# Kernel tuning notes

Measured on AMD Instinct MI355X. Metric: run time of the kernel, lower is better.

## Reference

```python
import jax, jax.numpy as jnp
import numpy as np

B = 64            # batchSize
F_ENC = 2048      # encodedFeatureSize = 128 features * 16 bits
H = 8192          # hiddenLayerSize
C = 100           # numberOfClasses
K = 8             # numberOfSynapsesPerSegment
THR = K // 2      # segment activation threshold (majority of synapses active)
NSEG = 2          # numberOfSegmentsPerNeuron


def _make_synapse_matrix(key, n_neurons, prev_size):
    # exactly K random synapses per neuron, values +1/-1 with equal prob
    k_idx, k_val = jax.random.split(key)
    cols = jax.random.randint(k_idx, (n_neurons, K), 0, prev_size)
    vals = jnp.where(jax.random.bernoulli(k_val, 0.5, (n_neurons, K)), 1.0, -1.0).astype(jnp.float32)
    rows = jnp.arange(n_neurons)[:, None]
    W = jnp.zeros((n_neurons, prev_size), dtype=jnp.float32)
    return W.at[rows, cols].set(vals)


def setup_inputs() -> dict:
    key = jax.random.key(0)
    ks = jax.random.split(key, 16)
    # binary encoded input (thermometer/gray-coded bits); rand in [0,1), binarized in reference
    x = jax.random.uniform(ks[0], (B, F_ENC), dtype=jnp.float32)
    W0_s0 = _make_synapse_matrix(ks[1], H, F_ENC)
    W0_s1 = _make_synapse_matrix(ks[2], H, F_ENC)
    W1_s0 = _make_synapse_matrix(ks[3], H, H)
    W1_s1 = _make_synapse_matrix(ks[4], H, H)
    W2_s0 = _make_synapse_matrix(ks[5], H, H)
    W2_s1 = _make_synapse_matrix(ks[6], H, H)
    # trained (non-binary) output connection strengths, one matrix per hidden layer
    O0 = jax.random.uniform(ks[7], (H, C), dtype=jnp.float32)
    O1 = jax.random.uniform(ks[8], (H, C), dtype=jnp.float32)
    O2 = jax.random.uniform(ks[9], (H, C), dtype=jnp.float32)
    return {"x": x, "W0_s0": W0_s0, "W0_s1": W0_s1, "W1_s0": W1_s0, "W1_s1": W1_s1,
            "W2_s0": W2_s0, "W2_s1": W2_s1, "O0": O0, "O1": O1, "O2": O2}


def _layer(a, W_s0, W_s1):
    # per-segment integer-valued synaptic sums over binary activations; a neuron
    # fires if ANY segment reaches the activation threshold
    z0 = a @ W_s0.T  # [B, H]
    z1 = a @ W_s1.T
    fired = jnp.logical_or(z0 >= THR, z1 >= THR)
    return fired.astype(jnp.float32)


def reference(x, W0_s0, W0_s1, W1_s0, W1_s1, W2_s0, W2_s1, O0, O1, O2):
    a0 = (x > 0.5).astype(jnp.float32)          # encoded binary input bits [B, F_ENC]
    a1 = _layer(a0, W0_s0, W0_s1)               # [B, H]
    a2 = _layer(a1, W1_s0, W1_s1)               # [B, H]
    a3 = _layer(a2, W2_s0, W2_s1)               # [B, H]
    # class scores: sum of output connection strengths from all active hidden neurons
    logits = a1 @ O0 + a2 @ O1 + a3 @ O2        # [B, C]
    return logits
```

## Files before the change

kernel.cpp:

```cpp
#include <hip/hip_runtime.h>
#include <stdint.h>

#define BATCH 64
#define F_ENC 2048
#define HID 8192
#define NCLS 100
#define NMAT 6
#define EXTRA 9

typedef unsigned long long ull;
typedef uint32_t u32x4 __attribute__((ext_vector_type(4)));

__device__ __forceinline__ void scan_vec(u32x4 w, int vecIdx,
                                         unsigned* s_cnt, uint16_t* s_ent) {
  uint32_t vals[4] = {w[0], w[1], w[2], w[3]};
#pragma unroll
  for (int e = 0; e < 4; ++e) {
    uint32_t u = vals[e];
    if (u != 0u) {
      unsigned slot = atomicAdd(s_cnt, 1u);
      s_ent[slot & 15u] = (uint16_t)(((vecIdx << 2) + e) | ((u >> 31) << 15));
    }
  }
}

__global__ void __launch_bounds__(256) sparsify_pack_kernel(
    const uint32_t* __restrict__ W0a, const uint32_t* __restrict__ W0b,
    const uint32_t* __restrict__ W1a, const uint32_t* __restrict__ W1b,
    const uint32_t* __restrict__ W2a, const uint32_t* __restrict__ W2b,
    const float* __restrict__ x, ull* __restrict__ A0,
    float* __restrict__ out, uint16_t* __restrict__ entries) {
  if (blockIdx.x < 8) {
    int c = blockIdx.x * 256 + threadIdx.x;
    ull m = 0;
#pragma unroll
    for (int b = 0; b < BATCH; ++b)
      m |= (ull)(x[(size_t)b * F_ENC + c] > 0.5f) << b;
    A0[c] = m;
    return;
  }
  if (blockIdx.x == 8) {
    for (int i = threadIdx.x; i < BATCH * NCLS; i += 256) out[i] = 0.f;
    return;
  }
  int blk = blockIdx.x - EXTRA;
  int m = blk >> 13;
  int r = blk & (HID - 1);
  const uint32_t* Wbase;
  switch (m) {
    case 0: Wbase = W0a; break;
    case 1: Wbase = W0b; break;
    case 2: Wbase = W1a; break;
    case 3: Wbase = W1b; break;
    case 4: Wbase = W2a; break;
    default: Wbase = W2b; break;
  }
  const int cols = (m < 2) ? F_ENC : HID;
  const u32x4* row = (const u32x4*)(Wbase + (size_t)r * cols);

  __shared__ unsigned s_cnt;
  __shared__ uint16_t s_ent[16];
  if (threadIdx.x == 0) s_cnt = 0u;
  __syncthreads();

  if (cols == F_ENC) {
    u32x4 w0 = __builtin_nontemporal_load(row + threadIdx.x);
    u32x4 w1 = __builtin_nontemporal_load(row + threadIdx.x + 256);
    asm volatile("" ::: "memory");
    uint32_t any = w0[0] | w0[1] | w0[2] | w0[3] |
                   w1[0] | w1[1] | w1[2] | w1[3];
    if (any) {
      scan_vec(w0, threadIdx.x, &s_cnt, s_ent);
      scan_vec(w1, threadIdx.x + 256, &s_cnt, s_ent);
    }
  } else {
    u32x4 w[8];
#pragma unroll
    for (int e = 0; e < 8; ++e)
      w[e] = __builtin_nontemporal_load(row + threadIdx.x + (e << 8));
    asm volatile("" ::: "memory");
    uint32_t any = 0;
#pragma unroll
    for (int e = 0; e < 8; ++e) any |= w[e][0] | w[e][1] | w[e][2] | w[e][3];
    if (any) {
#pragma unroll
      for (int e = 0; e < 8; ++e)
        scan_vec(w[e], threadIdx.x + (e << 8), &s_cnt, s_ent);
    }
  }
  __syncthreads();
  if (threadIdx.x < 8) {
    unsigned cnt = s_cnt;
    uint16_t v = (threadIdx.x < cnt) ? s_ent[threadIdx.x] : (uint16_t)0xFFFF;
    entries[(size_t)blk * 8 + threadIdx.x] = v;
  }
}

struct BS4 { ull p0, p1, p2, p3; };

__device__ __forceinline__ void bs_add(BS4& a, ull m) {
  ull c = m, t;
  t = a.p0 ^ c; c &= a.p0; a.p0 = t;
  t = a.p1 ^ c; c &= a.p1; a.p1 = t;
  t = a.p2 ^ c; c &= a.p2; a.p2 = t;
  a.p3 ^= c;
}

__device__ __forceinline__ ull bs_fired(const BS4& A, const BS4& Mn) {
  ull b0 = Mn.p0, b1 = Mn.p1;
  ull carry = Mn.p2;
  ull b2 = ~Mn.p2;
  ull b3 = Mn.p3 ^ carry;
  ull b4 = Mn.p3 & carry;
  ull res = 0, eq = ~0ull;
  eq &= ~b4;
  res |= eq & A.p3 & ~b3; eq &= ~(A.p3 ^ b3);
  res |= eq & A.p2 & ~b2; eq &= ~(A.p2 ^ b2);
  res |= eq & A.p1 & ~b1; eq &= ~(A.p1 ^ b1);
  res |= eq & A.p0 & ~b0; eq &= ~(A.p0 ^ b0);
  return res | eq;
}

__device__ __forceinline__ ull layer_fire(const uint16_t* __restrict__ ent0,
                                          const uint16_t* __restrict__ ent1,
                                          const ull* __restrict__ Aprev,
                                          int h) {
  uint4 p0 = ((const uint4*)ent0)[h];
  uint4 p1 = ((const uint4*)ent1)[h];
  uint32_t wd[8] = {p0.x, p0.y, p0.z, p0.w, p1.x, p1.y, p1.z, p1.w};
  uint16_t es[16];
#pragma unroll
  for (int i = 0; i < 8; ++i) {
    es[2 * i]     = (uint16_t)(wd[i] & 0xFFFFu);
    es[2 * i + 1] = (uint16_t)(wd[i] >> 16);
  }
  ull M[16];
#pragma unroll
  for (int i = 0; i < 16; ++i) {
    int idx = (es[i] == 0xFFFF) ? 0 : (es[i] & 0x1FFF);
    ull v = Aprev[idx];
    M[i] = (es[i] == 0xFFFF) ? 0ull : v;
  }
  ull f = 0;
#pragma unroll
  for (int s = 0; s < 2; ++s) {
    BS4 P{0, 0, 0, 0}, N{0, 0, 0, 0};
#pragma unroll
    for (int i = 0; i < 8; ++i) {
      uint16_t e = es[s * 8 + i];
      ull Mm = M[s * 8 + i];
      ull mp = (e & 0x8000) ? 0ull : Mm;
      ull mn = (e & 0x8000) ? Mm : 0ull;
      bs_add(P, mp);
      bs_add(N, mn);
    }
    f |= bs_fired(P, N);
  }
  return f;
}

__global__ void __launch_bounds__(256) layer_kernel(
    const uint16_t* __restrict__ ent0, const uint16_t* __restrict__ ent1,
    const ull* __restrict__ Aprev, ull* __restrict__ Anext) {
  int h = blockIdx.x * blockDim.x + threadIdx.x;
  if (h >= HID) return;
  Anext[h] = layer_fire(ent0, ent1, Aprev, h);
}

__global__ void __launch_bounds__(256) logits_kernel(
    const uint16_t* __restrict__ ent4, const uint16_t* __restrict__ ent5,
    const ull* __restrict__ A1, const ull* __restrict__ A2,
    const float* __restrict__ O0, const float* __restrict__ O1,
    const float* __restrict__ O2, float* __restrict__ out) {
  __shared__ float acc[BATCH * NCLS];
  __shared__ ull sA3[32];
  const int h0 = blockIdx.x * 32;
  if (threadIdx.x < 32)
    sA3[threadIdx.x] = layer_fire(ent4, ent5, A2, h0 + threadIdx.x);
  for (int i = threadIdx.x; i < BATCH * NCLS; i += 256) acc[i] = 0.f;
  __syncthreads();
  const int half = threadIdx.x >> 7;
  const int j = threadIdx.x & 127;
  if (j < NCLS) {
    const int bofs = half * 32;
    const int sh = half * 32;
    for (int k = 0; k < 32; ++k) {
      int h = h0 + k;
      uint32_t m1 = (uint32_t)(A1[h] >> sh);
      uint32_t m2 = (uint32_t)(A2[h] >> sh);
      uint32_t m3 = (uint32_t)(sA3[k] >> sh);
      if (m1) {
        float o = O0[(size_t)h * NCLS + j];
        do { int b = __builtin_ctz(m1); m1 &= m1 - 1; acc[(b + bofs) * NCLS + j] += o; } while (m1);
      }
      if (m2) {
        float o = O1[(size_t)h * NCLS + j];
        do { int b = __builtin_ctz(m2); m2 &= m2 - 1; acc[(b + bofs) * NCLS + j] += o; } while (m2);
      }
      if (m3) {
        float o = O2[(size_t)h * NCLS + j];
        do { int b = __builtin_ctz(m3); m3 &= m3 - 1; acc[(b + bofs) * NCLS + j] += o; } while (m3);
      }
    }
  }
  __syncthreads();
  for (int i = threadIdx.x; i < BATCH * NCLS; i += 256)
    atomicAdd(&out[i], acc[i]);
}

extern "C" void kernel_launch(void* const* d_in, const int* in_sizes, int n_in,
                              void* d_out, int out_size, void* d_ws, size_t ws_size,
                              hipStream_t stream) {
  const float*    x   = (const float*)d_in[0];
  const uint32_t* W0a = (const uint32_t*)d_in[1];
  const uint32_t* W0b = (const uint32_t*)d_in[2];
  const uint32_t* W1a = (const uint32_t*)d_in[3];
  const uint32_t* W1b = (const uint32_t*)d_in[4];
  const uint32_t* W2a = (const uint32_t*)d_in[5];
  const uint32_t* W2b = (const uint32_t*)d_in[6];
  const float*    O0  = (const float*)d_in[7];
  const float*    O1  = (const float*)d_in[8];
  const float*    O2  = (const float*)d_in[9];
  float* out = (float*)d_out;
  char*  ws  = (char*)d_ws;

  ull* A0 = (ull*)(ws);
  ull* A1 = (ull*)(ws + 16384);
  ull* A2 = (ull*)(ws + 16384 + 65536);
  uint16_t* entries = (uint16_t*)(ws + 16384 + 2 * 65536);

  sparsify_pack_kernel<<<EXTRA + NMAT * HID, 256, 0, stream>>>(
      W0a, W0b, W1a, W1b, W2a, W2b, x, A0, out, entries);
  layer_kernel<<<HID / 256, 256, 0, stream>>>(
      entries + (size_t)0 * HID * 8, entries + (size_t)1 * HID * 8, A0, A1);
  layer_kernel<<<HID / 256, 256, 0, stream>>>(
      entries + (size_t)2 * HID * 8, entries + (size_t)3 * HID * 8, A1, A2);
  logits_kernel<<<HID / 32, 256, 0, stream>>>(
      entries + (size_t)4 * HID * 8, entries + (size_t)5 * HID * 8,
      A1, A2, O0, O1, O2, out);
}
```

Before: 213.6 us.

## Fuse hidden layers and logits into one kernel with redundant per-block LDS recompute

Replaces the two layer kernels and the logits kernel with one fused kernel. Every block recomputes the full A1 and A2 bit-sliced activations into shared memory, then computes its own slice of A3 and accumulates logits from LDS-resident masks. This removes two kernel launches and the global round trips for A1/A2. In exchange, the layer compute and the entry reads from L2 are repeated in every one of the 256 blocks. The ~154KB of LDS per block also limits occupancy to one block per CU.

```diff
diff --git a/kernel.cpp b/kernel.cpp
--- a/kernel.cpp
+++ b/kernel.cpp
@@ -123,8 +123,7 @@
 
 __device__ __forceinline__ ull layer_fire(const uint16_t* __restrict__ ent0,
                                           const uint16_t* __restrict__ ent1,
-                                          const ull* __restrict__ Aprev,
-                                          int h) {
+                                          const ull* Aprev, int h) {
   uint4 p0 = ((const uint4*)ent0)[h];
   uint4 p1 = ((const uint4*)ent1)[h];
   uint32_t wd[8] = {p0.x, p0.y, p0.z, p0.w, p1.x, p1.y, p1.z, p1.w};
@@ -159,26 +158,42 @@
   return f;
 }
 
-__global__ void __launch_bounds__(256) layer_kernel(
-    const uint16_t* __restrict__ ent0, const uint16_t* __restrict__ ent1,
-    const ull* __restrict__ Aprev, ull* __restrict__ Anext) {
-  int h = blockIdx.x * blockDim.x + threadIdx.x;
-  if (h >= HID) return;
-  Anext[h] = layer_fire(ent0, ent1, Aprev, h);
-}
-
-__global__ void __launch_bounds__(256) logits_kernel(
-    const uint16_t* __restrict__ ent4, const uint16_t* __restrict__ ent5,
-    const ull* __restrict__ A1, const ull* __restrict__ A2,
+__global__ void __launch_bounds__(256) fused_tail_kernel(
+    const uint16_t* __restrict__ entries, const ull* __restrict__ A0,
     const float* __restrict__ O0, const float* __restrict__ O1,
     const float* __restrict__ O2, float* __restrict__ out) {
+  __shared__ ull sA1[HID];
+  __shared__ ull sA2[HID];
   __shared__ float acc[BATCH * NCLS];
   __shared__ ull sA3[32];
+
+  const uint16_t* ent0 = entries + (size_t)0 * HID * 8;
+  const uint16_t* ent1 = entries + (size_t)1 * HID * 8;
+  const uint16_t* ent2 = entries + (size_t)2 * HID * 8;
+  const uint16_t* ent3 = entries + (size_t)3 * HID * 8;
+  const uint16_t* ent4 = entries + (size_t)4 * HID * 8;
+  const uint16_t* ent5 = entries + (size_t)5 * HID * 8;
+
+#pragma unroll 4
+  for (int k = 0; k < 32; ++k) {
+    int h = threadIdx.x + k * 256;
+    sA1[h] = layer_fire(ent0, ent1, A0, h);
+  }
+  for (int i = threadIdx.x; i < BATCH * NCLS; i += 256) acc[i] = 0.f;
+  __syncthreads();
+
+#pragma unroll 4
+  for (int k = 0; k < 32; ++k) {
+    int h = threadIdx.x + k * 256;
+    sA2[h] = layer_fire(ent2, ent3, sA1, h);
+  }
+  __syncthreads();
+
   const int h0 = blockIdx.x * 32;
   if (threadIdx.x < 32)
-    sA3[threadIdx.x] = layer_fire(ent4, ent5, A2, h0 + threadIdx.x);
-  for (int i = threadIdx.x; i < BATCH * NCLS; i += 256) acc[i] = 0.f;
-  __syncthreads();
+    sA3[threadIdx.x] = layer_fire(ent4, ent5, sA2, h0 + threadIdx.x);
+  __syncthreads();
+
   const int half = threadIdx.x >> 7;
   const int j = threadIdx.x & 127;
   if (j < NCLS) {
@@ -186,8 +201,8 @@
     const int sh = half * 32;
     for (int k = 0; k < 32; ++k) {
       int h = h0 + k;
-      uint32_t m1 = (uint32_t)(A1[h] >> sh);
-      uint32_t m2 = (uint32_t)(A2[h] >> sh);
+      uint32_t m1 = (uint32_t)(sA1[h] >> sh);
+      uint32_t m2 = (uint32_t)(sA2[h] >> sh);
       uint32_t m3 = (uint32_t)(sA3[k] >> sh);
       if (m1) {
         float o = O0[(size_t)h * NCLS + j];
@@ -225,17 +240,10 @@
   char*  ws  = (char*)d_ws;
 
   ull* A0 = (ull*)(ws);
-  ull* A1 = (ull*)(ws + 16384);
-  ull* A2 = (ull*)(ws + 16384 + 65536);
-  uint16_t* entries = (uint16_t*)(ws + 16384 + 2 * 65536);
+  uint16_t* entries = (uint16_t*)(ws + 16384);
 
   sparsify_pack_kernel<<<EXTRA + NMAT * HID, 256, 0, stream>>>(
       W0a, W0b, W1a, W1b, W2a, W2b, x, A0, out, entries);
-  layer_kernel<<<HID / 256, 256, 0, stream>>>(
-      entries + (size_t)0 * HID * 8, entries + (size_t)1 * HID * 8, A0, A1);
-  layer_kernel<<<HID / 256, 256, 0, stream>>>(
-      entries + (size_t)2 * HID * 8, entries + (size_t)3 * HID * 8, A1, A2);
-  logits_kernel<<<HID / 32, 256, 0, stream>>>(
-      entries + (size_t)4 * HID * 8, entries + (size_t)5 * HID * 8,
-      A1, A2, O0, O1, O2, out);
-}
+  fused_tail_kernel<<<HID / 32, 256, 0, stream>>>(entries, A0, O0, O1, O2,
+                                                  out);
+}
```

Result: slower. 305.5 us (+43.0%).
